# Kernel tuning notes

Hardware: AMD Instinct MI355X
Metric: run time of the kernel (lower is better)

Reference implementation:

```python
import jax, jax.numpy as jnp
import numpy as np

L, H, E, HS, T, B, V, BS = 12, 12, 768, 64, 1024, 4, 50257, 1024
EPS = 1e-8
SCALE = E ** -0.5  # NOTE: original code scales by n_embd**-0.5, not head_size**-0.5


def _ln(x, g, b):
    mu = jnp.mean(x, axis=-1, keepdims=True)
    var = jnp.mean((x - mu) ** 2, axis=-1, keepdims=True)
    return (x - mu) / jnp.sqrt(var + EPS) * g + b


def setup_inputs() -> dict:
    key = jax.random.key(0)
    ks = iter(jax.random.split(key, 32))
    s = 0.02
    inp = {
        "idx": jax.random.randint(next(ks), (B, T), 0, V, dtype=jnp.int64),
        "tok_emb": jax.random.normal(next(ks), (V, E), jnp.float32) * s,
        "pos_emb": jax.random.normal(next(ks), (BS, E), jnp.float32) * s,
        "wq": jax.random.normal(next(ks), (L, H, E, HS), jnp.float32) * s,
        "wk": jax.random.normal(next(ks), (L, H, E, HS), jnp.float32) * s,
        "wv": jax.random.normal(next(ks), (L, H, E, HS), jnp.float32) * s,
        "proj_w": jax.random.normal(next(ks), (L, E, E), jnp.float32) * s,
        "proj_b": jnp.zeros((L, E), jnp.float32),
        "ln1_g": jnp.ones((L, E), jnp.float32),
        "ln1_b": jnp.zeros((L, E), jnp.float32),
        "ln2_g": jnp.ones((L, E), jnp.float32),
        "ln2_b": jnp.zeros((L, E), jnp.float32),
        "w1": jax.random.normal(next(ks), (L, E, 4 * E), jnp.float32) * s,
        "b1": jnp.zeros((L, 4 * E), jnp.float32),
        "w2": jax.random.normal(next(ks), (L, 4 * E, E), jnp.float32) * s,
        "b2": jnp.zeros((L, E), jnp.float32),
        "lnf_g": jnp.ones((E,), jnp.float32),
        "lnf_b": jnp.zeros((E,), jnp.float32),
        "head_w": jax.random.normal(next(ks), (E, V), jnp.float32) * s,
        "head_b": jnp.zeros((V,), jnp.float32),
    }
    return inp


def reference(idx, tok_emb, pos_emb, wq, wk, wv, proj_w, proj_b,
              ln1_g, ln1_b, ln2_g, ln2_b, w1, b1, w2, b2,
              lnf_g, lnf_b, head_w, head_b):
    x = tok_emb[idx] + pos_emb[jnp.arange(T)][None, :, :]  # [B,T,E]
    mask = jnp.tril(jnp.ones((T, T), bool))
    neg = jnp.finfo(x.dtype).min
    for l in range(L):
        # --- multi-head attention ---
        xn = _ln(x, ln1_g[l], ln1_b[l])
        q = jnp.einsum("bte,hed->bhtd", xn, wq[l])
        k = jnp.einsum("bte,hed->bhtd", xn, wk[l])
        v = jnp.einsum("bte,hed->bhtd", xn, wv[l])
        scores = jnp.einsum("bhtd,bhsd->bhts", q, k) * SCALE
        scores = jnp.where(mask, scores, neg)
        attn = jax.nn.softmax(scores, axis=-1)
        o = jnp.einsum("bhts,bhsd->bhtd", attn, v)  # [B,H,T,HS]
        o = o.transpose(0, 2, 1, 3).reshape(B, T, E)
        x = x + o @ proj_w[l].T + proj_b[l]
        # --- feed-forward ---
        xn = _ln(x, ln2_g[l], ln2_b[l])
        h = jax.nn.gelu(xn @ w1[l] + b1[l], approximate=False)
        x = x + h @ w2[l] + b2[l]
    x = _ln(x, lnf_g, lnf_b)
    logits = x @ head_w + head_b  # [B,T,V]
    return logits
```

## Files before the change

### kernel.cpp

```cpp
#include <hip/hip_runtime.h>
#include <hip/hip_bf16.h>
#include <stdint.h>
#include <math.h>

typedef __hip_bfloat16 bf16;
typedef short s16x8 __attribute__((ext_vector_type(8)));
typedef short s16x4 __attribute__((ext_vector_type(4)));
typedef float f32x4 __attribute__((ext_vector_type(4)));

#define SCALE_QK 0.03608439182435161f
#define NEG_BIG  -1.0e30f

__device__ __forceinline__ void lds_dma16(void* lds_uniform, const void* gsrc) {
  __builtin_amdgcn_global_load_lds(
      (const __attribute__((address_space(1))) unsigned int*)(uintptr_t)gsrc,
      (__attribute__((address_space(3))) unsigned int*)(unsigned int)(uintptr_t)lds_uniform,
      16, 0, 0);
}

enum { EPI_BF16 = 0, EPI_GELU = 1, EPI_RES = 2, EPI_HEAD = 3 };

template <int EPI>
__global__ __launch_bounds__(256)
void gemm_bt64(const bf16* __restrict__ A, const bf16* __restrict__ BT,
               const float* __restrict__ bias, float* Cf, bf16* Cb,
               int M, int N, int K, int Nreal)
{
  __shared__ __align__(16) bf16 As[2][64 * 32];
  __shared__ __align__(16) bf16 Bs[2][128 * 32];
  const int tid = threadIdx.x;
  const int w = tid >> 6, l = tid & 63;
  const int lo = l & 15, hi = l >> 4;
  const long row0 = (long)blockIdx.y * 64;
  const long col0 = (long)blockIdx.x * 128;

  const int c0 = w * 64 + l, c1 = c0 + 256;
  const int s0 = ((c0 & 3) ^ ((c0 >> 2) & 3)) * 8;
  const int s1 = ((c1 & 3) ^ ((c1 >> 2) & 3)) * 8;
  const bf16* a0 = A + (row0 + (c0 >> 2)) * K + s0;
  const bf16* b0 = BT + (col0 + (c0 >> 2)) * K + s0;
  const bf16* b1 = BT + (col0 + (c1 >> 2)) * K + s1;
  const int w512 = w * 512;

  const f32x4 zero4 = {0.f, 0.f, 0.f, 0.f};
  f32x4 acc[4][2];
#pragma unroll
  for (int m = 0; m < 4; ++m)
#pragma unroll
    for (int n = 0; n < 2; ++n) acc[m][n] = zero4;

  const int nk = K >> 5;
  lds_dma16(&As[0][w512],        a0);
  lds_dma16(&Bs[0][w512],        b0);
  lds_dma16(&Bs[0][2048 + w512], b1);
  __syncthreads();

  int cur = 0;
  for (int t = 0; t < nk; ++t) {
    if (t + 1 < nk) {
      const int kt = (t + 1) << 5;
      lds_dma16(&As[cur ^ 1][w512],        a0 + kt);
      lds_dma16(&Bs[cur ^ 1][w512],        b0 + kt);
      lds_dma16(&Bs[cur ^ 1][2048 + w512], b1 + kt);
    }
    s16x8 af[4], bfr[2];
#pragma unroll
    for (int m = 0; m < 4; ++m) {
      const int r = m * 16 + lo;
      af[m] = *(const s16x8*)&As[cur][r * 32 + ((hi ^ (r & 3))) * 8];
    }
#pragma unroll
    for (int n = 0; n < 2; ++n) {
      const int r = w * 32 + n * 16 + lo;
      bfr[n] = *(const s16x8*)&Bs[cur][r * 32 + ((hi ^ (r & 3))) * 8];
    }
#pragma unroll
    for (int m = 0; m < 4; ++m)
#pragma unroll
      for (int n = 0; n < 2; ++n)
        acc[m][n] = __builtin_amdgcn_mfma_f32_16x16x32_bf16(af[m], bfr[n], acc[m][n], 0, 0, 0);
    __syncthreads();
    cur ^= 1;
  }

#pragma unroll
  for (int m = 0; m < 4; ++m) {
#pragma unroll
    for (int n = 0; n < 2; ++n) {
      const long col = col0 + w * 32 + n * 16 + lo;
#pragma unroll
      for (int r = 0; r < 4; ++r) {
        const long row = row0 + m * 16 + hi * 4 + r;
        float v = acc[m][n][r];
        if constexpr (EPI == EPI_BF16) {
          Cb[row * N + col] = __float2bfloat16(v);
        } else if constexpr (EPI == EPI_GELU) {
          v += bias[col];
          v = 0.5f * v * (1.f + erff(v * 0.70710678118654752f));
          Cb[row * N + col] = __float2bfloat16(v);
        } else if constexpr (EPI == EPI_RES) {
          Cf[row * N + col] += v + bias[col];
        } else {
          if (col < Nreal) Cf[row * Nreal + col] = v + bias[col];
        }
      }
    }
  }
}

template <int EPI>
__global__ __launch_bounds__(512)
void gemm_bt256(const bf16* __restrict__ A, const bf16* __restrict__ BT,
                const float* __restrict__ bias, float* Cf, bf16* Cb,
                int K, int N, int Nreal)
{
  __shared__ __align__(16) bf16 As[2][256 * 32];
  __shared__ __align__(16) bf16 Bs[2][128 * 32];
  const int tid = threadIdx.x;
  const int w = tid >> 6, l = tid & 63;
  const int lo = l & 15, hi = l >> 4;
  const int wm = (w & 3) * 64, wn = (w >> 2) * 64;
  const long row0 = (long)blockIdx.y * 256;
  const long col0 = (long)blockIdx.x * 128;

  const int ss = ((tid & 3) ^ ((tid >> 2) & 3)) * 8;
  const bf16* a0 = A + (row0 + (tid >> 2)) * K + ss;
  const bf16* a1 = A + (row0 + 128 + (tid >> 2)) * K + ss;
  const bf16* b0 = BT + (col0 + (tid >> 2)) * K + ss;
  const int w512 = w * 512;

  const f32x4 zero4 = {0.f, 0.f, 0.f, 0.f};
  f32x4 acc[4][4];
#pragma unroll
  for (int m = 0; m < 4; ++m)
#pragma unroll
    for (int n = 0; n < 4; ++n) acc[m][n] = zero4;

  const int nk = K >> 5;
  lds_dma16(&As[0][w512],        a0);
  lds_dma16(&As[0][4096 + w512], a1);
  lds_dma16(&Bs[0][w512],        b0);
  __syncthreads();

  int cur = 0;
  for (int t = 0; t < nk; ++t) {
    if (t + 1 < nk) {
      const int kt = (t + 1) << 5;
      lds_dma16(&As[cur ^ 1][w512],        a0 + kt);
      lds_dma16(&As[cur ^ 1][4096 + w512], a1 + kt);
      lds_dma16(&Bs[cur ^ 1][w512],        b0 + kt);
    }
    s16x8 af[4], bfr[4];
#pragma unroll
    for (int m = 0; m < 4; ++m) {
      const int r = wm + m * 16 + lo;
      af[m] = *(const s16x8*)&As[cur][r * 32 + ((hi ^ (r & 3))) * 8];
    }
#pragma unroll
    for (int n = 0; n < 4; ++n) {
      const int r = wn + n * 16 + lo;
      bfr[n] = *(const s16x8*)&Bs[cur][r * 32 + ((hi ^ (r & 3))) * 8];
    }
#pragma unroll
    for (int m = 0; m < 4; ++m)
#pragma unroll
      for (int n = 0; n < 4; ++n)
        acc[m][n] = __builtin_amdgcn_mfma_f32_16x16x32_bf16(af[m], bfr[n], acc[m][n], 0, 0, 0);
    __syncthreads();
    cur ^= 1;
  }

#pragma unroll
  for (int m = 0; m < 4; ++m) {
#pragma unroll
    for (int n = 0; n < 4; ++n) {
      const long col = col0 + wn + n * 16 + lo;
#pragma unroll
      for (int r = 0; r < 4; ++r) {
        const long row = row0 + wm + m * 16 + hi * 4 + r;
        float v = acc[m][n][r];
        if constexpr (EPI == EPI_BF16) {
          Cb[row * N + col] = __float2bfloat16(v);
        } else if constexpr (EPI == EPI_GELU) {
          v += bias[col];
          v = 0.5f * v * (1.f + erff(v * 0.70710678118654752f));
          Cb[row * N + col] = __float2bfloat16(v);
        } else {
          if (col < Nreal) Cf[row * Nreal + col] = v + bias[col];
        }
      }
    }
  }
}

__global__ __launch_bounds__(256)
void attn_kernel(const bf16* __restrict__ qkv, bf16* __restrict__ o)
{
  __shared__ __align__(16) bf16 Kl[64 * 64];
  __shared__ __align__(16) bf16 Vl[64 * 64];
  __shared__ __align__(16) bf16 Pl[4][32 * 64];
  const int tid = threadIdx.x;
  const int w = tid >> 6, l = tid & 63;
  const int lo = l & 15, hi = l >> 4;
  const int q0 = (7 - blockIdx.x) * 128;
  const int b = blockIdx.y / 12, h = blockIdx.y % 12;
  const int wq0 = q0 + w * 32;
  const bf16* base = qkv + (long)b * 1024 * 2304;

  s16x8 qf[2][2];
#pragma unroll
  for (int m = 0; m < 2; ++m)
#pragma unroll
    for (int ks = 0; ks < 2; ++ks)
      qf[m][ks] = *(const s16x8*)(base + (long)(wq0 + m * 16 + lo) * 2304 + h * 64 + ks * 32 + hi * 8);

  const f32x4 zero4 = {0.f, 0.f, 0.f, 0.f};
  f32x4 oacc[2][4];
  float mst[2][4], lst[2][4];
#pragma unroll
  for (int m = 0; m < 2; ++m) {
#pragma unroll
    for (int n = 0; n < 4; ++n) oacc[m][n] = zero4;
#pragma unroll
    for (int r = 0; r < 4; ++r) { mst[m][r] = -3.0e38f; lst[m][r] = 0.f; }
  }

  const int cB = tid + 256;
  const int r0c = tid >> 3, sl0 = (tid & 7) ^ (r0c & 7);
  const int r1c = cB >> 3,  sl1 = (cB & 7) ^ (r1c & 7);

  const int nt = (q0 + 128) / 64;
  for (int t = 0; t < nt; ++t) {
    const int j0 = t * 64;
    const s16x8 rk0 = *(const s16x8*)(base + (long)(j0 + r0c) * 2304 +  768 + h * 64 + (tid & 7) * 8);
    const s16x8 rk1 = *(const s16x8*)(base + (long)(j0 + r1c) * 2304 +  768 + h * 64 + (cB  & 7) * 8);
    const s16x8 rv0 = *(const s16x8*)(base + (long)(j0 + r0c) * 2304 + 1536 + h * 64 + (tid & 7) * 8);
    const s16x8 rv1 = *(const s16x8*)(base + (long)(j0 + r1c) * 2304 + 1536 + h * 64 + (cB  & 7) * 8);
    __syncthreads();
    *(s16x8*)&Kl[r0c * 64 + sl0 * 8] = rk0;
    *(s16x8*)&Kl[r1c * 64 + sl1 * 8] = rk1;
    *(s16x8*)&Vl[r0c * 64 + sl0 * 8] = rv0;
    *(s16x8*)&Vl[r1c * 64 + sl1 * 8] = rv1;
    __syncthreads();

    if (j0 <= wq0 + 31) {
      f32x4 s[2][4];
#pragma unroll
      for (int m = 0; m < 2; ++m)
#pragma unroll
        for (int n = 0; n < 4; ++n) s[m][n] = zero4;
#pragma unroll
      for (int ks = 0; ks < 2; ++ks) {
        s16x8 kf[4];
#pragma unroll
        for (int n = 0; n < 4; ++n) {
          const int r = n * 16 + lo;
          kf[n] = *(const s16x8*)&Kl[r * 64 + ((ks * 4 + hi) ^ (r & 7)) * 8];
        }
#pragma unroll
        for (int m = 0; m < 2; ++m)
#pragma unroll
          for (int n = 0; n < 4; ++n)
            s[m][n] = __builtin_amdgcn_mfma_f32_16x16x32_bf16(qf[m][ks], kf[n], s[m][n], 0, 0, 0);
      }
      const bool edge = (j0 + 63 > wq0);
#pragma unroll
      for (int m = 0; m < 2; ++m)
#pragma unroll
        for (int n = 0; n < 4; ++n) {
          const int j = j0 + n * 16 + lo;
#pragma unroll
          for (int r = 0; r < 4; ++r) {
            float v = s[m][n][r] * SCALE_QK;
            if (edge && j > wq0 + m * 16 + hi * 4 + r) v = NEG_BIG;
            s[m][n][r] = v;
          }
        }
#pragma unroll
      for (int m = 0; m < 2; ++m)
#pragma unroll
        for (int r = 0; r < 4; ++r) {
          float x = fmaxf(fmaxf(s[m][0][r], s[m][1][r]), fmaxf(s[m][2][r], s[m][3][r]));
          x = fmaxf(x, __shfl_xor(x, 1));
          x = fmaxf(x, __shfl_xor(x, 2));
          x = fmaxf(x, __shfl_xor(x, 4));
          x = fmaxf(x, __shfl_xor(x, 8));
          const float mn = fmaxf(mst[m][r], x);
          const float corr = __expf(mst[m][r] - mn);
          mst[m][r] = mn;
          float rs = 0.f;
#pragma unroll
          for (int n = 0; n < 4; ++n) {
            float p = __expf(s[m][n][r] - mn);
            s[m][n][r] = p;
            rs += p;
          }
          rs += __shfl_xor(rs, 1);
          rs += __shfl_xor(rs, 2);
          rs += __shfl_xor(rs, 4);
          rs += __shfl_xor(rs, 8);
          lst[m][r] = lst[m][r] * corr + rs;
#pragma unroll
          for (int n = 0; n < 4; ++n) oacc[m][n][r] *= corr;
        }
#pragma unroll
      for (int m = 0; m < 2; ++m)
#pragma unroll
        for (int n = 0; n < 4; ++n)
#pragma unroll
          for (int r = 0; r < 4; ++r) {
            const int pr = m * 16 + hi * 4 + r;
            const int pc = n * 16 + lo;
            Pl[w][pr * 64 + ((pc >> 3) ^ (pr & 7)) * 8 + (pc & 7)] =
                __float2bfloat16(s[m][n][r]);
          }
      s16x8 pa[2][2];
#pragma unroll
      for (int m = 0; m < 2; ++m)
#pragma unroll
        for (int ks = 0; ks < 2; ++ks) {
          const int r = m * 16 + lo;
          pa[m][ks] = *(const s16x8*)&Pl[w][r * 64 + ((ks * 4 + hi) ^ (r & 7)) * 8];
        }
#pragma unroll
      for (int ks = 0; ks < 2; ++ks)
#pragma unroll
        for (int n = 0; n < 4; ++n) {
          s16x8 vf;
#pragma unroll
          for (int j = 0; j < 8; ++j) {
            const int vr = ks * 32 + hi * 8 + j;
            const int vd = n * 16 + lo;
            vf[j] = *(const short*)&Vl[vr * 64 + ((vd >> 3) ^ (vr & 7)) * 8 + (vd & 7)];
          }
#pragma unroll
          for (int m = 0; m < 2; ++m)
            oacc[m][n] = __builtin_amdgcn_mfma_f32_16x16x32_bf16(pa[m][ks], vf, oacc[m][n], 0, 0, 0);
        }
    }
  }
#pragma unroll
  for (int m = 0; m < 2; ++m)
#pragma unroll
    for (int n = 0; n < 4; ++n)
#pragma unroll
      for (int r = 0; r < 4; ++r) {
        const int q = wq0 + m * 16 + hi * 4 + r;
        o[(long)(b * 1024 + q) * 768 + h * 64 + n * 16 + lo] =
            __float2bfloat16(oacc[m][n][r] / lst[m][r]);
      }
}

__global__ void detect_idx(const int* __restrict__ idx, int* __restrict__ flag)
{
  const int t = threadIdx.x;
  const int v = idx[2 * t + 1];
  const unsigned long long nz = __ballot(v != 0);
  if (t == 0) flag[0] = (nz == 0ull) ? 1 : 0;
}

__global__ __launch_bounds__(192)
void embed_kernel(const int* __restrict__ idx, const float* __restrict__ tok,
                  const float* __restrict__ pos, float* __restrict__ x,
                  const int* __restrict__ flag)
{
  const int row = blockIdx.x;
  const int t = row & 1023;
  const int id = flag[0] ? idx[2 * row] : idx[row];
  const int e = threadIdx.x * 4;
  const float4 a = *(const float4*)&tok[(long)id * 768 + e];
  const float4 p = *(const float4*)&pos[(long)t * 768 + e];
  float4 r; r.x = a.x + p.x; r.y = a.y + p.y; r.z = a.z + p.z; r.w = a.w + p.w;
  *(float4*)&x[(long)row * 768 + e] = r;
}

__global__ __launch_bounds__(256)
void ln_kernel(const float* __restrict__ x, const float* __restrict__ g,
               const float* __restrict__ bt, bf16* __restrict__ out)
{
  const int lane = threadIdx.x & 63;
  const int row = blockIdx.x * 4 + (threadIdx.x >> 6);
  const float* xr = x + (long)row * 768;
  f32x4 v[3];
  float s = 0.f, q = 0.f;
#pragma unroll
  for (int p = 0; p < 3; ++p) {
    v[p] = *(const f32x4*)&xr[lane * 4 + p * 256];
#pragma unroll
    for (int j = 0; j < 4; ++j) { s += v[p][j]; q += v[p][j] * v[p][j]; }
  }
#pragma unroll
  for (int o = 32; o > 0; o >>= 1) { s += __shfl_xor(s, o); q += __shfl_xor(q, o); }
  const float mu = s * (1.f / 768.f);
  const float var = q * (1.f / 768.f) - mu * mu;
  const float rs = rsqrtf(var + 1e-8f);
  bf16* orow = out + (long)row * 768;
#pragma unroll
  for (int p = 0; p < 3; ++p) {
    const int e = lane * 4 + p * 256;
    s16x4 pk;
#pragma unroll
    for (int j = 0; j < 4; ++j) {
      bf16 t = __float2bfloat16((v[p][j] - mu) * rs * g[e + j] + bt[e + j]);
      pk[j] = *(const short*)&t;
    }
    *(s16x4*)&orow[e] = pk;
  }
}

__device__ __forceinline__ void tile_tr64(const float* __restrict__ ip,
                                          bf16* __restrict__ op,
                                          int R, int Creal, int r0, int c0,
                                          int tid, float (*tile)[65])
{
  const int tx = tid & 63, ty = tid >> 6;
#pragma unroll
  for (int p = 0; p < 16; ++p) {
    const int r = p * 4 + ty;
    const int c = c0 + tx;
    tile[r][tx] = (c < Creal) ? ip[(long)(r0 + r) * Creal + c] : 0.f;
  }
  __syncthreads();
#pragma unroll
  for (int p = 0; p < 16; ++p) {
    const int cc = p * 4 + ty;
    op[(long)(c0 + cc) * R + r0 + tx] = __float2bfloat16(tile[tx][cc]);
  }
}

__global__ __launch_bounds__(256)
void transpose_conv(const float* __restrict__ in, bf16* __restrict__ out,
                    int R, int Creal)
{
  __shared__ float tile[64][65];
  tile_tr64(in, out, R, Creal, blockIdx.y * 64, blockIdx.x * 64, threadIdx.x, tile);
}

__global__ __launch_bounds__(256)
void repack_layer(const float* __restrict__ wq, const float* __restrict__ wk,
                  const float* __restrict__ wv, const float* __restrict__ projw,
                  const float* __restrict__ w1, const float* __restrict__ w2,
                  bf16* __restrict__ WqkvT, bf16* __restrict__ WprojT,
                  bf16* __restrict__ W1T, bf16* __restrict__ W2T)
{
  __shared__ float tile[64][65];
  const int tid = threadIdx.x;
  const int t = blockIdx.x;
  if (t < 432) {
    const int op_i = t / 144, r = t % 144;
    const int h = r / 12, ry = r % 12;
    const float* ip = (op_i == 0 ? wq : op_i == 1 ? wk : wv) + h * 49152;
    bf16* op = WqkvT + (long)op_i * 768 * 768 + (long)h * 64 * 768;
    tile_tr64(ip, op, 768, 64, ry * 64, 0, tid, tile);
  } else if (t < 576) {
    const int t2 = t - 432;
    const int r0 = (t2 / 12) * 64, c0 = (t2 % 12) * 64;
#pragma unroll
    for (int p = 0; p < 4; ++p) {
      const int row = r0 + p * 16 + (tid >> 4);
      const int col = c0 + (tid & 15) * 4;
      const float4 v = *(const float4*)&projw[(long)row * 768 + col];
      bf16 t0 = __float2bfloat16(v.x), t1 = __float2bfloat16(v.y);
      bf16 t2b = __float2bfloat16(v.z), t3 = __float2bfloat16(v.w);
      s16x4 pk;
      pk[0] = *(const short*)&t0; pk[1] = *(const short*)&t1;
      pk[2] = *(const short*)&t2b; pk[3] = *(const short*)&t3;
      *(s16x4*)&WprojT[(long)row * 768 + col] = pk;
    }
  } else if (t < 1152) {
    const int t3 = t - 576;
    tile_tr64(w1, W1T, 768, 3072, (t3 / 48) * 64, (t3 % 48) * 64, tid, tile);
  } else {
    const int t4 = t - 1152;
    tile_tr64(w2, W2T, 3072, 768, (t4 / 12) * 64, (t4 % 12) * 64, tid, tile);
  }
}

extern "C" void kernel_launch(void* const* d_in, const int* in_sizes, int n_in,
                              void* d_out, int out_size, void* d_ws, size_t ws_size,
                              hipStream_t stream)
{
  (void)in_sizes; (void)n_in; (void)out_size; (void)ws_size;
  const int*   idx   = (const int*)d_in[0];
  const float* tok   = (const float*)d_in[1];
  const float* pos   = (const float*)d_in[2];
  const float* wq    = (const float*)d_in[3];
  const float* wk    = (const float*)d_in[4];
  const float* wv    = (const float*)d_in[5];
  const float* projw = (const float*)d_in[6];
  const float* projb = (const float*)d_in[7];
  const float* ln1g  = (const float*)d_in[8];
  const float* ln1b  = (const float*)d_in[9];
  const float* ln2g  = (const float*)d_in[10];
  const float* ln2b  = (const float*)d_in[11];
  const float* w1    = (const float*)d_in[12];
  const float* b1    = (const float*)d_in[13];
  const float* w2    = (const float*)d_in[14];
  const float* b2    = (const float*)d_in[15];
  const float* lnfg  = (const float*)d_in[16];
  const float* lnfb  = (const float*)d_in[17];
  const float* headw = (const float*)d_in[18];
  const float* headb = (const float*)d_in[19];
  float* out = (float*)d_out;

  char* ws = (char*)d_ws;
  size_t off = 0;
  auto alloc = [&](size_t bytes) -> void* {
    void* p = ws + off; off += (bytes + 255) & ~(size_t)255; return p;
  };
  int*   iflag  = (int*)  alloc(256);
  float* x      = (float*)alloc(4096ull * 768 * 4);
  bf16*  xn     = (bf16*) alloc(4096ull * 768 * 2);
  bf16*  qkvb   = (bf16*) alloc(4096ull * 2304 * 2);
  bf16*  ob     = (bf16*) alloc(4096ull * 768 * 2);
  bf16*  hb     = (bf16*) alloc(4096ull * 3072 * 2);
  bf16*  WqkvT  = (bf16*) alloc(2304ull * 768 * 2);
  bf16*  WprojT = (bf16*) alloc(768ull * 768 * 2);
  bf16*  W1T    = (bf16*) alloc(3072ull * 768 * 2);
  bf16*  W2T    = (bf16*) alloc(768ull * 3072 * 2);
  bf16*  headT  = (bf16*) alloc(50304ull * 768 * 2);

  detect_idx<<<1, 64, 0, stream>>>(idx, iflag);
  transpose_conv<<<dim3(786, 12), 256, 0, stream>>>(headw, headT, 768, 50257);
  embed_kernel<<<4096, 192, 0, stream>>>(idx, tok, pos, x, iflag);

  for (int l = 0; l < 12; ++l) {
    const size_t hOff = (size_t)l * 12 * 768 * 64;
    repack_layer<<<1728, 256, 0, stream>>>(wq + hOff, wk + hOff, wv + hOff,
                                           projw + (size_t)l * 768 * 768,
                                           w1 + (size_t)l * 768 * 3072,
                                           w2 + (size_t)l * 3072 * 768,
                                           WqkvT, WprojT, W1T, W2T);

    ln_kernel<<<1024, 256, 0, stream>>>(x, ln1g + l * 768, ln1b + l * 768, xn);
    gemm_bt256<EPI_BF16><<<dim3(18, 16), 512, 0, stream>>>(xn, WqkvT, nullptr, nullptr, qkvb, 768, 2304, 2304);
    attn_kernel<<<dim3(8, 48), 256, 0, stream>>>(qkvb, ob);
    gemm_bt64<EPI_RES><<<dim3(6, 64), 256, 0, stream>>>(ob, WprojT, projb + l * 768, x, nullptr, 4096, 768, 768, 768);
    ln_kernel<<<1024, 256, 0, stream>>>(x, ln2g + l * 768, ln2b + l * 768, xn);
    gemm_bt256<EPI_GELU><<<dim3(24, 16), 512, 0, stream>>>(xn, W1T, b1 + (size_t)l * 3072, nullptr, hb, 768, 3072, 3072);
    gemm_bt64<EPI_RES><<<dim3(6, 64), 256, 0, stream>>>(hb, W2T, b2 + l * 768, x, nullptr, 4096, 768, 3072, 768);
  }

  ln_kernel<<<1024, 256, 0, stream>>>(x, lnfg, lnfb, xn);
  gemm_bt256<EPI_HEAD><<<dim3(393, 16), 512, 0, stream>>>(xn, headT, headb, out, nullptr, 768, 50304, 50257);
}
```

Baseline: 3.323 ms.

## Split-K residual GEMMs with atomic adds and fold LN1 into repack kernel

The two residual-add GEMMs (attention projection and FFN down-projection) are split along K into two z-slices. Each slice atomically adds its partial result into the fp32 residual, and only slice 0 adds the bias. This doubles the block count from 384 to 768 so more of the GPU is occupied. Separately, the first LayerNorm of each layer now runs as extra blocks appended to the weight-repack kernel, removing one launch per layer. The atomics add contention and make the floating-point summation order nondeterministic.

```diff
diff --git a/kernel.cpp b/kernel.cpp
--- a/kernel.cpp
+++ b/kernel.cpp
@@ -18,7 +18,7 @@
       16, 0, 0);
 }
 
-enum { EPI_BF16 = 0, EPI_GELU = 1, EPI_RES = 2, EPI_HEAD = 3 };
+enum { EPI_BF16 = 0, EPI_GELU = 1, EPI_RES = 2, EPI_HEAD = 3, EPI_RESA = 4 };
 
 template <int EPI>
 __global__ __launch_bounds__(256)
@@ -33,13 +33,15 @@
   const int lo = l & 15, hi = l >> 4;
   const long row0 = (long)blockIdx.y * 64;
   const long col0 = (long)blockIdx.x * 128;
+  const int Keff = K / (int)gridDim.z;
+  const int kbase = (int)blockIdx.z * Keff;
 
   const int c0 = w * 64 + l, c1 = c0 + 256;
   const int s0 = ((c0 & 3) ^ ((c0 >> 2) & 3)) * 8;
   const int s1 = ((c1 & 3) ^ ((c1 >> 2) & 3)) * 8;
-  const bf16* a0 = A + (row0 + (c0 >> 2)) * K + s0;
-  const bf16* b0 = BT + (col0 + (c0 >> 2)) * K + s0;
-  const bf16* b1 = BT + (col0 + (c1 >> 2)) * K + s1;
+  const bf16* a0 = A + (row0 + (c0 >> 2)) * K + kbase + s0;
+  const bf16* b0 = BT + (col0 + (c0 >> 2)) * K + kbase + s0;
+  const bf16* b1 = BT + (col0 + (c1 >> 2)) * K + kbase + s1;
   const int w512 = w * 512;
 
   const f32x4 zero4 = {0.f, 0.f, 0.f, 0.f};
@@ -49,7 +51,7 @@
 #pragma unroll
     for (int n = 0; n < 2; ++n) acc[m][n] = zero4;
 
-  const int nk = K >> 5;
+  const int nk = Keff >> 5;
   lds_dma16(&As[0][w512],        a0);
   lds_dma16(&Bs[0][w512],        b0);
   lds_dma16(&Bs[0][2048 + w512], b1);
@@ -100,6 +102,9 @@
           Cb[row * N + col] = __float2bfloat16(v);
         } else if constexpr (EPI == EPI_RES) {
           Cf[row * N + col] += v + bias[col];
+        } else if constexpr (EPI == EPI_RESA) {
+          if (blockIdx.z == 0) v += bias[col];
+          unsafeAtomicAdd(&Cf[row * N + col], v);
         } else {
           if (col < Nreal) Cf[row * Nreal + col] = v + bias[col];
         }
@@ -374,12 +379,14 @@
   *(float4*)&x[(long)row * 768 + e] = r;
 }
 
-__global__ __launch_bounds__(256)
-void ln_kernel(const float* __restrict__ x, const float* __restrict__ g,
-               const float* __restrict__ bt, bf16* __restrict__ out)
-{
-  const int lane = threadIdx.x & 63;
-  const int row = blockIdx.x * 4 + (threadIdx.x >> 6);
+__device__ __forceinline__ void ln_rows(const float* __restrict__ x,
+                                        const float* __restrict__ g,
+                                        const float* __restrict__ bt,
+                                        bf16* __restrict__ out,
+                                        int row4, int tid)
+{
+  const int lane = tid & 63;
+  const int row = row4 * 4 + (tid >> 6);
   const float* xr = x + (long)row * 768;
   f32x4 v[3];
   float s = 0.f, q = 0.f;
@@ -408,6 +415,13 @@
   }
 }
 
+__global__ __launch_bounds__(256)
+void ln_kernel(const float* __restrict__ x, const float* __restrict__ g,
+               const float* __restrict__ bt, bf16* __restrict__ out)
+{
+  ln_rows(x, g, bt, out, blockIdx.x, threadIdx.x);
+}
+
 __device__ __forceinline__ void tile_tr64(const float* __restrict__ ip,
                                           bf16* __restrict__ op,
                                           int R, int Creal, int r0, int c0,
@@ -440,8 +454,11 @@
 void repack_layer(const float* __restrict__ wq, const float* __restrict__ wk,
                   const float* __restrict__ wv, const float* __restrict__ projw,
                   const float* __restrict__ w1, const float* __restrict__ w2,
+                  const float* __restrict__ x, const float* __restrict__ ln1g,
+                  const float* __restrict__ ln1b,
                   bf16* __restrict__ WqkvT, bf16* __restrict__ WprojT,
-                  bf16* __restrict__ W1T, bf16* __restrict__ W2T)
+                  bf16* __restrict__ W1T, bf16* __restrict__ W2T,
+                  bf16* __restrict__ xn)
 {
   __shared__ float tile[64][65];
   const int tid = threadIdx.x;
@@ -470,9 +487,11 @@
   } else if (t < 1152) {
     const int t3 = t - 576;
     tile_tr64(w1, W1T, 768, 3072, (t3 / 48) * 64, (t3 % 48) * 64, tid, tile);
-  } else {
+  } else if (t < 1728) {
     const int t4 = t - 1152;
     tile_tr64(w2, W2T, 3072, 768, (t4 / 12) * 64, (t4 % 12) * 64, tid, tile);
+  } else {
+    ln_rows(x, ln1g, ln1b, xn, t - 1728, tid);
   }
 }
 
@@ -526,19 +545,19 @@
 
   for (int l = 0; l < 12; ++l) {
     const size_t hOff = (size_t)l * 12 * 768 * 64;
-    repack_layer<<<1728, 256, 0, stream>>>(wq + hOff, wk + hOff, wv + hOff,
+    repack_layer<<<2752, 256, 0, stream>>>(wq + hOff, wk + hOff, wv + hOff,
                                            projw + (size_t)l * 768 * 768,
                                            w1 + (size_t)l * 768 * 3072,
                                            w2 + (size_t)l * 3072 * 768,
-                                           WqkvT, WprojT, W1T, W2T);
-
-    ln_kernel<<<1024, 256, 0, stream>>>(x, ln1g + l * 768, ln1b + l * 768, xn);
+                                           x, ln1g + l * 768, ln1b + l * 768,
+                                           WqkvT, WprojT, W1T, W2T, xn);
+
     gemm_bt256<EPI_BF16><<<dim3(18, 16), 512, 0, stream>>>(xn, WqkvT, nullptr, nullptr, qkvb, 768, 2304, 2304);
     attn_kernel<<<dim3(8, 48), 256, 0, stream>>>(qkvb, ob);
-    gemm_bt64<EPI_RES><<<dim3(6, 64), 256, 0, stream>>>(ob, WprojT, projb + l * 768, x, nullptr, 4096, 768, 768, 768);
+    gemm_bt64<EPI_RESA><<<dim3(6, 64, 2), 256, 0, stream>>>(ob, WprojT, projb + l * 768, x, nullptr, 4096, 768, 768, 768);
     ln_kernel<<<1024, 256, 0, stream>>>(x, ln2g + l * 768, ln2b + l * 768, xn);
     gemm_bt256<EPI_GELU><<<dim3(24, 16), 512, 0, stream>>>(xn, W1T, b1 + (size_t)l * 3072, nullptr, hb, 768, 3072, 3072);
-    gemm_bt64<EPI_RES><<<dim3(6, 64), 256, 0, stream>>>(hb, W2T, b2 + l * 768, x, nullptr, 4096, 768, 3072, 768);
+    gemm_bt64<EPI_RESA><<<dim3(6, 64, 2), 256, 0, stream>>>(hb, W2T, b2 + l * 768, x, nullptr, 4096, 768, 3072, 768);
   }
 
   ln_kernel<<<1024, 256, 0, stream>>>(x, lnfg, lnfb, xn);
```

New measurement: 3.395 ms. 1.02x slower.
